# Kernel optimization log

Hardware: AMD Instinct MI355X
Metric: run time of the kernel (lower is better)

The kernel has to match this reference:

```python
import jax, jax.numpy as jnp
import numpy as np

N, E, H, L, IN, OUT = 50000, 600000, 128, 4, 10, 3
EPS = 1e-5

def _ln(x, g, b):
    m = jnp.mean(x, axis=-1, keepdims=True)
    v = jnp.mean(jnp.square(x - m), axis=-1, keepdims=True)
    return (x - m) * jax.lax.rsqrt(v + EPS) * g + b

def _mlp(x, w1, b1, w2, b2, g, be):
    h = jax.nn.relu(x @ w1 + b1)
    return _ln(h @ w2 + b2, g, be)

def setup_inputs() -> dict:
    key = jax.random.key(0)
    ks = iter(jax.random.split(key, 40))
    def w(shape, fan_in):
        return jax.random.normal(next(ks), shape, jnp.float32) * (1.0 / np.sqrt(fan_in))
    inp = {
        'x': jax.random.normal(next(ks), (N, IN), jnp.float32),
        'edge_index': jax.random.randint(next(ks), (2, E), 0, N, jnp.int32),
        'edge_attr': jax.random.normal(next(ks), (E, 3), jnp.float32),
        'enc_w1': w((IN, H), IN), 'enc_b1': jnp.zeros((H,), jnp.float32),
        'enc_w2': w((H, H), H), 'enc_b2': jnp.zeros((H,), jnp.float32),
        'enc_g': jnp.ones((H,), jnp.float32), 'enc_be': jnp.zeros((H,), jnp.float32),
        'edge_w1': w((L, 2 * H + 3, H), 2 * H + 3), 'edge_b1': jnp.zeros((L, H), jnp.float32),
        'edge_w2': w((L, H, H), H), 'edge_b2': jnp.zeros((L, H), jnp.float32),
        'edge_g': jnp.ones((L, H), jnp.float32), 'edge_be': jnp.zeros((L, H), jnp.float32),
        'node_w1': w((L, 2 * H, H), 2 * H), 'node_b1': jnp.zeros((L, H), jnp.float32),
        'node_w2': w((L, H, H), H), 'node_b2': jnp.zeros((L, H), jnp.float32),
        'node_g': jnp.ones((L, H), jnp.float32), 'node_be': jnp.zeros((L, H), jnp.float32),
        'dec_w1': w((H, H), H), 'dec_b1': jnp.zeros((H,), jnp.float32),
        'dec_w2': w((H, OUT), H), 'dec_b2': jnp.zeros((OUT,), jnp.float32),
    }
    return inp

def reference(x, edge_index, edge_attr,
              enc_w1, enc_b1, enc_w2, enc_b2, enc_g, enc_be,
              edge_w1, edge_b1, edge_w2, edge_b2, edge_g, edge_be,
              node_w1, node_b1, node_w2, node_b2, node_g, node_be,
              dec_w1, dec_b1, dec_w2, dec_b2):
    src, tgt = edge_index[0], edge_index[1]  # x_j = h[src], x_i = h[tgt]
    h = _mlp(x, enc_w1, enc_b1, enc_w2, enc_b2, enc_g, enc_be)  # [N,H]
    for l in range(L):
        x_i, x_j = h[tgt], h[src]                               # [E,H] gathers
        msg_in = jnp.concatenate([x_i, x_j, edge_attr], axis=1)  # [E,2H+3]
        msg = _mlp(msg_in, edge_w1[l], edge_b1[l], edge_w2[l], edge_b2[l], edge_g[l], edge_be[l])
        aggr = jax.ops.segment_sum(msg, tgt, num_segments=h.shape[0])  # [N,H]
        upd_in = jnp.concatenate([h, aggr], axis=1)              # [N,2H]
        h = h + _mlp(upd_in, node_w1[l], node_b1[l], node_w2[l], node_b2[l], node_g[l], node_be[l])
    out = jax.nn.relu(h @ dec_w1 + dec_b1) @ dec_w2 + dec_b2     # [N,OUT]
    return out
```

## Files before the change

kernel.cpp:

```cpp
#include <hip/hip_runtime.h>

#define H 128
#define LPAD 132
#define BM 64

typedef __attribute__((ext_vector_type(8))) short bf8;
typedef __attribute__((ext_vector_type(4))) float f4;
typedef __attribute__((ext_vector_type(4))) short s4;

__device__ __forceinline__ short f2bf(float f) {
    unsigned u = __float_as_uint(f);
    unsigned r = u + 0x7FFFu + ((u >> 16) & 1u);
    return (short)(r >> 16);
}
__device__ __forceinline__ float bf2f(unsigned lo16) {
    return __uint_as_float((lo16 & 0xFFFFu) << 16);
}

__global__ void pack_w(const float* __restrict__ W, short* __restrict__ out, int K, int KC) {
    const int layer = blockIdx.z;
    const float* Wl = W + (size_t)layer * K * H;
    short* ol = out + (size_t)layer * 8 * KC * 512;
    const int total = 8 * KC * 512;
    for (int idx = blockIdx.x * blockDim.x + threadIdx.x; idx < total; idx += gridDim.x * blockDim.x) {
        int i = idx & 7;
        int lane = (idx >> 3) & 63;
        int v = idx >> 9;
        int kc = v % KC;
        int m = v / KC;
        int k = kc * 32 + (lane >> 4) * 8 + i;
        int c = m * 16 + (lane & 15);
        float val = (k < K) ? Wl[(size_t)k * H + c] : 0.f;
        ol[idx] = f2bf(val);
    }
}

__global__ void pack_wts(const float* __restrict__ W , short* __restrict__ out) {
    const int layer = blockIdx.z;
    const float* Wl = W + (size_t)layer * 259 * 128;
    short* ol = out + (size_t)layer * 16 * 4 * 512;
    const int total = 16 * 4 * 512;
    for (int idx = blockIdx.x * blockDim.x + threadIdx.x; idx < total; idx += gridDim.x * blockDim.x) {
        int i = idx & 7;
        int lane = (idx >> 3) & 63;
        int v = idx >> 9;
        int kc = v & 3;
        int m = v >> 2;
        int k = kc * 32 + (lane >> 4) * 8 + i;
        int c = m * 16 + (lane & 15);
        float val = (c < 128) ? Wl[(size_t)k * 128 + c] : Wl[(size_t)(128 + k) * 128 + (c - 128)];
        ol[idx] = f2bf(val);
    }
}

__global__ void csr_count(const int* __restrict__ tgt, int* __restrict__ cnt, int E) {
    int e = blockIdx.x * blockDim.x + threadIdx.x;
    if (e < E) atomicAdd(&cnt[tgt[e]], 1);
}

#define SCAN_T 1024
__global__ __launch_bounds__(SCAN_T) void scan_excl(const int* __restrict__ cnt,
                                                    int* __restrict__ start, int n) {
    __shared__ int part[SCAN_T];
    int t = threadIdx.x;
    int chunk = (n + SCAN_T - 1) / SCAN_T;
    int lo = t * chunk, hi = min(lo + chunk, n);
    int s = 0;
    for (int i = lo; i < hi; ++i) s += cnt[i];
    part[t] = s;
    __syncthreads();
    for (int off = 1; off < SCAN_T; off <<= 1) {
        int v = (t >= off) ? part[t - off] : 0;
        __syncthreads();
        part[t] += v;
        __syncthreads();
    }
    int base = (t > 0) ? part[t - 1] : 0;
    for (int i = lo; i < hi; ++i) { start[i] = base; base += cnt[i]; }
}

__global__ void csr_scatter_reorder(const int* __restrict__ tgtI, const int* __restrict__ srcI,
                                    const float* __restrict__ eattr,
                                    int* __restrict__ start,
                                    int2* __restrict__ stpair,
                                    short* __restrict__ attrb, int E) {
    int e = blockIdx.x * blockDim.x + threadIdx.x;
    if (e >= E) return;
    int t = tgtI[e];
    int p = atomicAdd(&start[t], 1);
    stpair[p] = make_int2(srcI[e], t);
    s4 vv = {};
    vv[0] = f2bf(eattr[(size_t)e * 3 + 0]);
    vv[1] = f2bf(eattr[(size_t)e * 3 + 1]);
    vv[2] = f2bf(eattr[(size_t)e * 3 + 2]);
    *(s4*)(attrb + (size_t)p * 4) = vv;
}

__global__ __launch_bounds__(512, 4) void ts_mfma(
    const short* __restrict__ hbf, const short* __restrict__ wtsp,
    const float* __restrict__ b1,
    short* __restrict__ Tarr, short* __restrict__ Sarr,
    float* __restrict__ aggr, int N) {
    __shared__ __align__(16) short sW[16 * 4 * 512];
    const int tid = threadIdx.x;
    for (int t = tid; t < 16 * 4 * 512 / 8; t += 512) ((uint4*)sW)[t] = ((const uint4*)wtsp)[t];
    __syncthreads();

    const int lane = tid & 63;
    const int wv = tid >> 6;
    const int g = lane >> 4;
    const int er = lane & 15;
    const int n = blockIdx.x * 128 + wv * 16 + er;
    const int nC = (n < N) ? n : 0;
    const bf8* rT = (const bf8*)(hbf + (size_t)nC * H);

    f4 acc[16] = {};
#pragma unroll
    for (int kc = 0; kc < 4; ++kc) {
        bf8 b = rT[kc * 4 + g];
#pragma unroll
        for (int m = 0; m < 16; ++m)
            acc[m] = __builtin_amdgcn_mfma_f32_16x16x32_bf16(
                *(const bf8*)(sW + ((m * 4 + kc) * 64 + lane) * 8), b, acc[m], 0, 0, 0);
    }
    if (n >= N) return;
    short* oT = Tarr + (size_t)n * 128;
    short* oS = Sarr + (size_t)n * 128;
    float* oZ = aggr + (size_t)n * 128;
    const f4 zz = {0.f, 0.f, 0.f, 0.f};
#pragma unroll
    for (int m = 0; m < 16; ++m) {
        f4 v = acc[m];
        if (m < 8) {
            f4 bb = *(const f4*)(b1 + m * 16 + 4 * g);
            v = v + bb;
            *(f4*)(oZ + m * 16 + 4 * g) = zz;
        }
        unsigned p0, p1;
        asm("v_cvt_pk_bf16_f32 %0, %1, %2" : "=v"(p0) : "v"(v[0]), "v"(v[1]));
        asm("v_cvt_pk_bf16_f32 %0, %1, %2" : "=v"(p1) : "v"(v[2]), "v"(v[3]));
        uint2 uu; uu.x = p0; uu.y = p1;
        if (m < 8) *(uint2*)(oT + m * 16 + 4 * g) = uu;
        else       *(uint2*)(oS + (m - 8) * 16 + 4 * g) = uu;
    }
}

__global__ __launch_bounds__(512, 4) void edge_fused(
    const short* __restrict__ Tarr, const short* __restrict__ Sarr,
    const short* __restrict__ attrbf,
    const int2* __restrict__ stpair,
    const short* __restrict__ w2p,
    const float* __restrict__ w1aG,
    const float* __restrict__ b2,
    const float* __restrict__ gamma, const float* __restrict__ beta,
    float* __restrict__ aggr, int nrows) {
    __shared__ __align__(16) short sW2[8 * 4 * 512];
    __shared__ float sw1a[3 * 128];
    __shared__ __align__(16) unsigned smsg[128 * 64];
    __shared__ int stgt[128];

    const int tid = threadIdx.x;
    for (int t = tid; t < 8 * 4 * 512 / 8; t += 512) ((uint4*)sW2)[t] = ((const uint4*)w2p)[t];
    if (tid < 384) sw1a[tid] = w1aG[tid];
    const int e0b = blockIdx.x * 128;
    if (tid < 128) {
        int ee = e0b + tid;
        stgt[tid] = (ee < nrows) ? stpair[ee].y : -1;
    }
    __syncthreads();

    const int lane = tid & 63;
    const int wv = tid >> 6;
    const int g = lane >> 4;
    const int er = lane & 15;
    const int le = wv * 16 + er;
    const int e = e0b + le;
    const bool valid = e < nrows;
    const int eC = valid ? e : 0;
    const int2 st = stpair[eC];
    const int tS = st.x;
    const int tT = st.y;

    uint2 au = *(const uint2*)(attrbf + (size_t)eC * 4);
    const float at0 = bf2f(au.x), at1 = bf2f(au.x >> 16), at2 = bf2f(au.y);

    const short* Tp = Tarr + (size_t)tT * 128;
    const short* Sp = Sarr + (size_t)tS * 128;

    f4 acc2[8] = {};
#pragma unroll
    for (int kc2 = 0; kc2 < 4; ++kc2) {
        const int c0 = kc2 * 32 + 8 * g;
        uint4 tu = *(const uint4*)(Tp + c0);
        uint4 su = *(const uint4*)(Sp + c0);
        unsigned tw[4] = {tu.x, tu.y, tu.z, tu.w};
        unsigned swd[4] = {su.x, su.y, su.z, su.w};
        float hv[8];
#pragma unroll
        for (int p = 0; p < 4; ++p) {
            int j0 = 2 * p;
            float t0 = bf2f(tw[p]), t1 = bf2f(tw[p] >> 16);
            float s0 = bf2f(swd[p]), s1 = bf2f(swd[p] >> 16);
            float a = t0 + s0 + at0 * sw1a[c0 + j0] + at1 * sw1a[128 + c0 + j0] + at2 * sw1a[256 + c0 + j0];
            hv[j0] = fmaxf(a, 0.f);
            float b = t1 + s1 + at0 * sw1a[c0 + j0 + 1] + at1 * sw1a[128 + c0 + j0 + 1] + at2 * sw1a[256 + c0 + j0 + 1];
            hv[j0 + 1] = fmaxf(b, 0.f);
        }
        bf8 bfr;
        unsigned* bu = (unsigned*)&bfr;
#pragma unroll
        for (int p = 0; p < 4; ++p)
            asm("v_cvt_pk_bf16_f32 %0, %1, %2" : "=v"(bu[p]) : "v"(hv[2 * p]), "v"(hv[2 * p + 1]));
#pragma unroll
        for (int m = 0; m < 8; ++m)
            acc2[m] = __builtin_amdgcn_mfma_f32_16x16x32_bf16(
                *(const bf8*)(sW2 + ((m * 4 + kc2) * 64 + lane) * 8), bfr, acc2[m], 0, 0, 0);
    }

    float o[8][4];
    float s = 0.f, q = 0.f;
#pragma unroll
    for (int m = 0; m < 8; ++m) {
        f4 bb = *(const f4*)(b2 + m * 16 + 4 * g);
#pragma unroll
        for (int r = 0; r < 4; ++r) {
            float v = acc2[m][r] + bb[r];
            o[m][r] = v; s += v; q += v * v;
        }
    }
    s += __shfl_xor(s, 16, 64); q += __shfl_xor(q, 16, 64);
    s += __shfl_xor(s, 32, 64); q += __shfl_xor(q, 32, 64);
    const float mean = s * (1.f / 128.f);
    const float inv = rsqrtf(q * (1.f / 128.f) - mean * mean + 1e-5f);

    const unsigned swz = (unsigned)((le & 7) << 3);
    unsigned* row = smsg + le * 64;
#pragma unroll
    for (int m = 0; m < 8; ++m) {
        f4 gg = *(const f4*)(gamma + m * 16 + 4 * g);
        f4 be4 = *(const f4*)(beta + m * 16 + 4 * g);
        float v0 = valid ? ((o[m][0] - mean) * inv * gg[0] + be4[0]) : 0.f;
        float v1 = valid ? ((o[m][1] - mean) * inv * gg[1] + be4[1]) : 0.f;
        float v2 = valid ? ((o[m][2] - mean) * inv * gg[2] + be4[2]) : 0.f;
        float v3 = valid ? ((o[m][3] - mean) * inv * gg[3] + be4[3]) : 0.f;
        unsigned p0, p1;
        asm("v_cvt_pk_bf16_f32 %0, %1, %2" : "=v"(p0) : "v"(v0), "v"(v1));
        asm("v_cvt_pk_bf16_f32 %0, %1, %2" : "=v"(p1) : "v"(v2), "v"(v3));
        unsigned d0 = ((unsigned)(m * 8 + 2 * g)) ^ swz;
        uint2 uu; uu.x = p0; uu.y = p1;
        *(uint2*)(row + d0) = uu;
    }
    __syncthreads();

    const int c2 = tid & 63;
    const int chunk = tid >> 6;
    float a0 = 0.f, a1 = 0.f;
    int cur = stgt[chunk * 16];
    for (int j = 0; j < 16; ++j) {
        int le2 = chunk * 16 + j;
        int tg = stgt[le2];
        if (tg != cur) {
            if (cur >= 0) {
                atomicAdd(&aggr[(size_t)cur * 128 + 2 * c2], a0);
                atomicAdd(&aggr[(size_t)cur * 128 + 2 * c2 + 1], a1);
            }
            a0 = 0.f; a1 = 0.f; cur = tg;
        }
        unsigned u = smsg[le2 * 64 + (c2 ^ ((le2 & 7) << 3))];
        a0 += __uint_as_float(u << 16);
        a1 += __uint_as_float(u & 0xFFFF0000u);
    }
    if (cur >= 0) {
        atomicAdd(&aggr[(size_t)cur * 128 + 2 * c2], a0);
        atomicAdd(&aggr[(size_t)cur * 128 + 2 * c2 + 1], a1);
    }
}

__global__ __launch_bounds__(1024, 4) void node_mfma(
    const short* __restrict__ hbf, const float* __restrict__ aggrf,
    const short* __restrict__ w1p, const short* __restrict__ w2p,
    const float* __restrict__ b1, const float* __restrict__ b2,
    const float* __restrict__ gamma, const float* __restrict__ beta,
    float* __restrict__ outp, short* __restrict__ hbfout, int nrows) {
    __shared__ __align__(16) short sW1[8 * 8 * 512];
    __shared__ __align__(16) short sW2[8 * 4 * 512];

    const int tid = threadIdx.x;
    for (int t = tid; t < 8 * 8 * 512 / 8; t += 1024) ((uint4*)sW1)[t] = ((const uint4*)w1p)[t];
    for (int t = tid; t < 8 * 4 * 512 / 8; t += 1024) ((uint4*)sW2)[t] = ((const uint4*)w2p)[t];
    __syncthreads();

    const int lane = tid & 63;
    const int wv = tid >> 6;
    const int g = lane >> 4;
    const int er = lane & 15;
    const int e = blockIdx.x * 256 + wv * 16 + er;
    const bool valid = e < nrows;
    const int eC = valid ? e : 0;

    const bf8* rT = (const bf8*)(hbf + (size_t)eC * H);
    const f4* ra = (const f4*)(aggrf + (size_t)eC * H);

    f4 acc1[8] = {};
#pragma unroll
    for (int kc = 0; kc < 4; ++kc) {
        bf8 b = rT[kc * 4 + g];
#pragma unroll
        for (int m = 0; m < 8; ++m)
            acc1[m] = __builtin_amdgcn_mfma_f32_16x16x32_bf16(
                *(const bf8*)(sW1 + ((m * 8 + kc) * 64 + lane) * 8), b, acc1[m], 0, 0, 0);
    }
#pragma unroll
    for (int kc = 4; kc < 8; ++kc) {
        f4 a0 = ra[(kc - 4) * 8 + g * 2];
        f4 a1 = ra[(kc - 4) * 8 + g * 2 + 1];
        bf8 b;
        unsigned* bu = (unsigned*)&b;
        asm("v_cvt_pk_bf16_f32 %0, %1, %2" : "=v"(bu[0]) : "v"(a0[0]), "v"(a0[1]));
        asm("v_cvt_pk_bf16_f32 %0, %1, %2" : "=v"(bu[1]) : "v"(a0[2]), "v"(a0[3]));
        asm("v_cvt_pk_bf16_f32 %0, %1, %2" : "=v"(bu[2]) : "v"(a1[0]), "v"(a1[1]));
        asm("v_cvt_pk_bf16_f32 %0, %1, %2" : "=v"(bu[3]) : "v"(a1[2]), "v"(a1[3]));
#pragma unroll
        for (int m = 0; m < 8; ++m)
            acc1[m] = __builtin_amdgcn_mfma_f32_16x16x32_bf16(
                *(const bf8*)(sW1 + ((m * 8 + kc) * 64 + lane) * 8), b, acc1[m], 0, 0, 0);
    }

    float h1[8][4];
#pragma unroll
    for (int m = 0; m < 8; ++m) {
        f4 bb = *(const f4*)(b1 + m * 16 + 4 * g);
#pragma unroll
        for (int r = 0; r < 4; ++r) h1[m][r] = fmaxf(acc1[m][r] + bb[r], 0.f);
    }

    unsigned pk[8][2];
#pragma unroll
    for (int m = 0; m < 8; ++m)
#pragma unroll
        for (int hh = 0; hh < 2; ++hh)
            asm("v_cvt_pk_bf16_f32 %0, %1, %2"
                : "=v"(pk[m][hh]) : "v"(h1[m][2 * hh]), "v"(h1[m][2 * hh + 1]));

    f4 acc2[8] = {};
#pragma unroll
    for (int kc2 = 0; kc2 < 4; ++kc2) {
        bf8 bfr;
        unsigned* bu = (unsigned*)&bfr;
#pragma unroll
        for (int p = 0; p < 4; ++p) {
            int sl = er + 16 * (2 * (g & 1) + (p >> 1));
            unsigned lo = (unsigned)__shfl((int)pk[2 * kc2 + 0][p & 1], sl, 64);
            unsigned hi = (unsigned)__shfl((int)pk[2 * kc2 + 1][p & 1], sl, 64);
            bu[p] = (g >> 1) ? hi : lo;
        }
#pragma unroll
        for (int m = 0; m < 8; ++m)
            acc2[m] = __builtin_amdgcn_mfma_f32_16x16x32_bf16(
                *(const bf8*)(sW2 + ((m * 4 + kc2) * 64 + lane) * 8), bfr, acc2[m], 0, 0, 0);
    }

    float o[8][4];
    float s = 0.f, q = 0.f;
#pragma unroll
    for (int m = 0; m < 8; ++m) {
        f4 bb = *(const f4*)(b2 + m * 16 + 4 * g);
#pragma unroll
        for (int r = 0; r < 4; ++r) {
            float v = acc2[m][r] + bb[r];
            o[m][r] = v; s += v; q += v * v;
        }
    }
    s += __shfl_xor(s, 16, 64); q += __shfl_xor(q, 16, 64);
    s += __shfl_xor(s, 32, 64); q += __shfl_xor(q, 32, 64);
    const float mean = s * (1.f / 128.f);
    const float inv = rsqrtf(q * (1.f / 128.f) - mean * mean + 1e-5f);

    if (!valid) return;
    float* hp = outp + (size_t)eC * H;
    short* hb = hbfout + (size_t)eC * H;
#pragma unroll
    for (int m = 0; m < 8; ++m) {
        f4 gg = *(const f4*)(gamma + m * 16 + 4 * g);
        f4 be4 = *(const f4*)(beta + m * 16 + 4 * g);
        f4 hv = *(const f4*)(hp + m * 16 + 4 * g);
        f4 nv; s4 pkk;
#pragma unroll
        for (int r = 0; r < 4; ++r) {
            nv[r] = hv[r] + (o[m][r] - mean) * inv * gg[r] + be4[r];
            pkk[r] = f2bf(nv[r]);
        }
        *(f4*)(hp + m * 16 + 4 * g) = nv;
        *(s4*)(hb + m * 16 + 4 * g) = pkk;
    }
}

enum { MODE_ENC = 0, MODE_DEC = 3 };

__device__ __forceinline__ void fma_row(float acc[4], float a, const float4& b) {
    acc[0] = fmaf(a, b.x, acc[0]);
    acc[1] = fmaf(a, b.y, acc[1]);
    acc[2] = fmaf(a, b.z, acc[2]);
    acc[3] = fmaf(a, b.w, acc[3]);
}

__device__ __forceinline__ void gemm_seg(const float (*A)[LPAD], int K,
                                         const float* __restrict__ B,
                                         int row0, int c0, float acc[8][4]) {
    int k = 0;
    for (; k + 4 <= K; k += 4) {
        float4 b0 = *(const float4*)(B + (size_t)(k + 0) * H + c0);
        float4 b1 = *(const float4*)(B + (size_t)(k + 1) * H + c0);
        float4 b2 = *(const float4*)(B + (size_t)(k + 2) * H + c0);
        float4 b3 = *(const float4*)(B + (size_t)(k + 3) * H + c0);
#pragma unroll
        for (int j = 0; j < 8; ++j) {
            float4 a = *(const float4*)(&A[row0 + j][k]);
            fma_row(acc[j], a.x, b0);
            fma_row(acc[j], a.y, b1);
            fma_row(acc[j], a.z, b2);
            fma_row(acc[j], a.w, b3);
        }
    }
    for (; k < K; ++k) {
        float4 bv = *(const float4*)(B + (size_t)k * H + c0);
#pragma unroll
        for (int j = 0; j < 8; ++j) fma_row(acc[j], A[row0 + j][k], bv);
    }
}

template <int MODE>
__global__ __launch_bounds__(256, 2) void mlp_small(
    const float* __restrict__ in0,
    const float* __restrict__ w1, const float* __restrict__ b1,
    const float* __restrict__ w2, const float* __restrict__ b2,
    const float* __restrict__ g, const float* __restrict__ be,
    float* __restrict__ outp, short* __restrict__ hbfout, int nrows) {
    __shared__ __align__(16) float sA[BM][LPAD];

    const int tid = threadIdx.x;
    const int tr = tid >> 5, tc = tid & 31;
    const int c0 = tc * 4, row0 = tr * 8;
    const int r0 = blockIdx.x * BM;

    if (MODE == MODE_ENC) {
        for (int idx = tid; idx < BM * 10; idx += 256) {
            int r = idx / 10, c = idx - 10 * (idx / 10);
            int n = r0 + r;
            sA[r][c] = (n < nrows) ? in0[(size_t)n * 10 + c] : 0.f;
        }
    } else {
        for (int idx = tid; idx < BM * 32; idx += 256) {
            int r = idx >> 5, qq = idx & 31;
            int n = r0 + r;
            float4 v0 = make_float4(0.f, 0.f, 0.f, 0.f);
            if (n < nrows) v0 = ((const float4*)in0)[(size_t)n * 32 + qq];
            *(float4*)&sA[r][qq * 4] = v0;
        }
    }
    __syncthreads();

    float acc[8][4];
    {
        float4 bb = *(const float4*)&b1[c0];
#pragma unroll
        for (int j = 0; j < 8; ++j) { acc[j][0] = bb.x; acc[j][1] = bb.y; acc[j][2] = bb.z; acc[j][3] = bb.w; }
    }
    gemm_seg(sA, (MODE == MODE_ENC) ? 10 : H, w1, row0, c0, acc);
#pragma unroll
    for (int j = 0; j < 8; ++j)
#pragma unroll
        for (int r = 0; r < 4; ++r) acc[j][r] = fmaxf(acc[j][r], 0.f);

    __syncthreads();
#pragma unroll
    for (int j = 0; j < 8; ++j)
        *(float4*)&sA[row0 + j][c0] = make_float4(acc[j][0], acc[j][1], acc[j][2], acc[j][3]);
    __syncthreads();

    if (MODE == MODE_DEC) {
        if (tid < BM * 3) {
            int r = tid / 3, o = tid - 3 * (tid / 3);
            int gr = r0 + r;
            float sv = b2[o];
            for (int i = 0; i < H; ++i) sv = fmaf(sA[r][i], w2[(size_t)i * 3 + o], sv);
            if (gr < nrows) outp[(size_t)gr * 3 + o] = sv;
        }
        return;
    }

    {
        float4 bb = *(const float4*)&b2[c0];
#pragma unroll
        for (int j = 0; j < 8; ++j) { acc[j][0] = bb.x; acc[j][1] = bb.y; acc[j][2] = bb.z; acc[j][3] = bb.w; }
    }
    gemm_seg(sA, H, w2, row0, c0, acc);

    float4 g4 = *(const float4*)&g[c0];
    float4 be4 = *(const float4*)&be[c0];
#pragma unroll
    for (int j = 0; j < 8; ++j) {
        float s = acc[j][0] + acc[j][1] + acc[j][2] + acc[j][3];
        float q = acc[j][0] * acc[j][0] + acc[j][1] * acc[j][1] +
                  acc[j][2] * acc[j][2] + acc[j][3] * acc[j][3];
#pragma unroll
        for (int m = 1; m < 32; m <<= 1) { s += __shfl_xor(s, m); q += __shfl_xor(q, m); }
        float mean = s * (1.0f / 128.0f);
        float inv = rsqrtf(q * (1.0f / 128.0f) - mean * mean + 1e-5f);
        int gr = r0 + row0 + j;
        if (gr >= nrows) continue;
        float v0 = (acc[j][0] - mean) * inv * g4.x + be4.x;
        float v1 = (acc[j][1] - mean) * inv * g4.y + be4.y;
        float v2 = (acc[j][2] - mean) * inv * g4.z + be4.z;
        float v3 = (acc[j][3] - mean) * inv * g4.w + be4.w;
        *(float4*)&outp[(size_t)gr * H + c0] = make_float4(v0, v1, v2, v3);
        s4 pk = {f2bf(v0), f2bf(v1), f2bf(v2), f2bf(v3)};
        *(s4*)&hbfout[(size_t)gr * H + c0] = pk;
    }
}

static inline size_t align16(size_t x) { return (x + 15) & ~(size_t)15; }

extern "C" void kernel_launch(void* const* d_in, const int* in_sizes, int n_in,
                              void* d_out, int out_size, void* d_ws, size_t ws_size,
                              hipStream_t stream) {
    const float* x       = (const float*)d_in[0];
    const int*   ei      = (const int*)d_in[1];
    const float* eattr   = (const float*)d_in[2];
    const float* enc_w1  = (const float*)d_in[3];
    const float* enc_b1  = (const float*)d_in[4];
    const float* enc_w2  = (const float*)d_in[5];
    const float* enc_b2  = (const float*)d_in[6];
    const float* enc_g   = (const float*)d_in[7];
    const float* enc_be  = (const float*)d_in[8];
    const float* edge_w1 = (const float*)d_in[9];
    const float* edge_b1 = (const float*)d_in[10];
    const float* edge_w2 = (const float*)d_in[11];
    const float* edge_b2 = (const float*)d_in[12];
    const float* edge_g  = (const float*)d_in[13];
    const float* edge_be = (const float*)d_in[14];
    const float* node_w1 = (const float*)d_in[15];
    const float* node_b1 = (const float*)d_in[16];
    const float* node_w2 = (const float*)d_in[17];
    const float* node_b2 = (const float*)d_in[18];
    const float* node_g  = (const float*)d_in[19];
    const float* node_be = (const float*)d_in[20];
    const float* dec_w1  = (const float*)d_in[21];
    const float* dec_b1  = (const float*)d_in[22];
    const float* dec_w2  = (const float*)d_in[23];
    const float* dec_b2  = (const float*)d_in[24];

    const int N = in_sizes[0] / 10;
    const int E = in_sizes[1] / 2;
    const int* srcI = ei;
    const int* tgtI = ei + E;

    char* base = (char*)d_ws;
    size_t off = 0;
    float* h     = (float*)(base + off); off = align16(off + (size_t)N * H * 4);
    float* aggr  = (float*)(base + off); off = align16(off + (size_t)N * H * 4);
    short* hbf   = (short*)(base + off); off = align16(off + (size_t)N * H * 2);
    short* Tarr  = (short*)(base + off); off = align16(off + (size_t)N * H * 2);
    short* Sarr  = (short*)(base + off); off = align16(off + (size_t)N * H * 2);
    short* attrb = (short*)(base + off); off = align16(off + (size_t)E * 4 * 2);
    short* ewtsp = (short*)(base + off); off = align16(off + (size_t)4 * 16 * 4 * 512 * 2);
    short* ew2p  = (short*)(base + off); off = align16(off + (size_t)4 * 8 * 4 * 512 * 2);
    short* nw1p  = (short*)(base + off); off = align16(off + (size_t)4 * 8 * 8 * 512 * 2);
    short* nw2p  = (short*)(base + off); off = align16(off + (size_t)4 * 8 * 4 * 512 * 2);
    int*   cnt   = (int*)(base + off);  off = align16(off + (size_t)N * 4);
    int*   startp= (int*)(base + off);  off = align16(off + (size_t)(N + 1) * 4);
    int2*  stpair= (int2*)(base + off); off = align16(off + (size_t)E * 8);

    pack_wts<<<dim3(64, 1, 4), 256, 0, stream>>>(edge_w1, ewtsp);
    pack_w<<<dim3(32, 1, 4), 256, 0, stream>>>(edge_w2, ew2p, H, 4);
    pack_w<<<dim3(64, 1, 4), 256, 0, stream>>>(node_w1, nw1p, 2 * H, 8);
    pack_w<<<dim3(32, 1, 4), 256, 0, stream>>>(node_w2, nw2p, H, 4);

    hipMemsetAsync(cnt, 0, (size_t)N * 4, stream);
    csr_count<<<(E + 255) / 256, 256, 0, stream>>>(tgtI, cnt, E);
    scan_excl<<<1, SCAN_T, 0, stream>>>(cnt, startp, N);
    csr_scatter_reorder<<<(E + 255) / 256, 256, 0, stream>>>(
        tgtI, srcI, eattr, startp, stpair, attrb, E);

    const int gN64 = (N + BM - 1) / BM;
    mlp_small<MODE_ENC><<<gN64, 256, 0, stream>>>(
        x, enc_w1, enc_b1, enc_w2, enc_b2, enc_g, enc_be, h, hbf, N);

    const int gTS = (N + 127) / 128;
    const int gEe = (E + 127) / 128;
    const int gNN = (N + 255) / 256;
    for (int l = 0; l < 4; ++l) {
        ts_mfma<<<gTS, 512, 0, stream>>>(
            hbf, ewtsp + (size_t)l * 16 * 4 * 512, edge_b1 + (size_t)l * H, Tarr, Sarr, aggr, N);
        const float* w1aG = edge_w1 + (size_t)l * 259 * 128 + 256 * 128;
        edge_fused<<<gEe, 512, 0, stream>>>(
            Tarr, Sarr, attrb, stpair, ew2p + (size_t)l * 8 * 4 * 512, w1aG,
            edge_b2 + (size_t)l * H, edge_g + (size_t)l * H, edge_be + (size_t)l * H,
            aggr, E);
        node_mfma<<<gNN, 1024, 0, stream>>>(
            hbf, aggr,
            nw1p + (size_t)l * 8 * 8 * 512, nw2p + (size_t)l * 8 * 4 * 512,
            node_b1 + (size_t)l * H, node_b2 + (size_t)l * H,
            node_g + (size_t)l * H, node_be + (size_t)l * H,
            h, hbf, N);
    }

    mlp_small<MODE_DEC><<<gN64, 256, 0, stream>>>(
        h, dec_w1, dec_b1, dec_w2, dec_b2, nullptr, nullptr, (float*)d_out, nullptr, N);
}
```

Baseline: 795.6 us.

## Fuse next-layer T/S projection into node update kernel, halve edge message LDS

The node update kernel now also computes the next layer's per-node source and target projections. It packs the new h in registers, reshuffles it into MFMA operand layout with lane shuffles, and writes Tarr/Sarr and zeroes aggr, which removes three separate ts_mfma launches and a re-read of hbf. The edge kernel's message staging buffer is halved by staging and reducing the 128 edges in two passes of 64 with an extra barrier, lowering LDS use to allow more occupancy. The trade-off is more registers in node_mfma and a race risk, because aggr is read and zeroed for the same rows within one thread.

Measured after the change: 895.7 us. 12.6% more time.

```diff
diff --git a/kernel.cpp b/kernel.cpp
--- a/kernel.cpp
+++ b/kernel.cpp
@@ -156,7 +156,7 @@
     float* __restrict__ aggr, int nrows) {
     __shared__ __align__(16) short sW2[8 * 4 * 512];
     __shared__ float sw1a[3 * 128];
-    __shared__ __align__(16) unsigned smsg[128 * 64];
+    __shared__ __align__(16) unsigned smsg[64 * 64];
     __shared__ int stgt[128];
 
     const int tid = threadIdx.x;
@@ -233,8 +233,7 @@
     const float mean = s * (1.f / 128.f);
     const float inv = rsqrtf(q * (1.f / 128.f) - mean * mean + 1e-5f);
 
-    const unsigned swz = (unsigned)((le & 7) << 3);
-    unsigned* row = smsg + le * 64;
+    unsigned pm[8][2];
 #pragma unroll
     for (int m = 0; m < 8; ++m) {
         f4 gg = *(const f4*)(gamma + m * 16 + 4 * g);
@@ -243,45 +242,61 @@
         float v1 = valid ? ((o[m][1] - mean) * inv * gg[1] + be4[1]) : 0.f;
         float v2 = valid ? ((o[m][2] - mean) * inv * gg[2] + be4[2]) : 0.f;
         float v3 = valid ? ((o[m][3] - mean) * inv * gg[3] + be4[3]) : 0.f;
-        unsigned p0, p1;
-        asm("v_cvt_pk_bf16_f32 %0, %1, %2" : "=v"(p0) : "v"(v0), "v"(v1));
-        asm("v_cvt_pk_bf16_f32 %0, %1, %2" : "=v"(p1) : "v"(v2), "v"(v3));
-        unsigned d0 = ((unsigned)(m * 8 + 2 * g)) ^ swz;
-        uint2 uu; uu.x = p0; uu.y = p1;
-        *(uint2*)(row + d0) = uu;
-    }
-    __syncthreads();
-
-    const int c2 = tid & 63;
-    const int chunk = tid >> 6;
-    float a0 = 0.f, a1 = 0.f;
-    int cur = stgt[chunk * 16];
-    for (int j = 0; j < 16; ++j) {
-        int le2 = chunk * 16 + j;
-        int tg = stgt[le2];
-        if (tg != cur) {
-            if (cur >= 0) {
-                atomicAdd(&aggr[(size_t)cur * 128 + 2 * c2], a0);
-                atomicAdd(&aggr[(size_t)cur * 128 + 2 * c2 + 1], a1);
+        asm("v_cvt_pk_bf16_f32 %0, %1, %2" : "=v"(pm[m][0]) : "v"(v0), "v"(v1));
+        asm("v_cvt_pk_bf16_f32 %0, %1, %2" : "=v"(pm[m][1]) : "v"(v2), "v"(v3));
+    }
+
+    const int myhalf = le >> 6;
+    const int rloc = le & 63;
+    const int c2 = lane;
+#pragma unroll
+    for (int hh = 0; hh < 2; ++hh) {
+        if (myhalf == hh) {
+            const unsigned swz = (unsigned)((rloc & 7) << 3);
+            unsigned* row = smsg + rloc * 64;
+#pragma unroll
+            for (int m = 0; m < 8; ++m) {
+                unsigned d0 = ((unsigned)(m * 8 + 2 * g)) ^ swz;
+                uint2 uu; uu.x = pm[m][0]; uu.y = pm[m][1];
+                *(uint2*)(row + d0) = uu;
             }
-            a0 = 0.f; a1 = 0.f; cur = tg;
-        }
-        unsigned u = smsg[le2 * 64 + (c2 ^ ((le2 & 7) << 3))];
-        a0 += __uint_as_float(u << 16);
-        a1 += __uint_as_float(u & 0xFFFF0000u);
-    }
-    if (cur >= 0) {
-        atomicAdd(&aggr[(size_t)cur * 128 + 2 * c2], a0);
-        atomicAdd(&aggr[(size_t)cur * 128 + 2 * c2 + 1], a1);
-    }
-}
-
+        }
+        __syncthreads();
+        float a0 = 0.f, a1 = 0.f;
+        int cur = stgt[hh * 64 + wv * 8];
+#pragma unroll
+        for (int j = 0; j < 8; ++j) {
+            int rl = wv * 8 + j;
+            int tg = stgt[hh * 64 + rl];
+            if (tg != cur) {
+                if (cur >= 0) {
+                    atomicAdd(&aggr[(size_t)cur * 128 + 2 * c2], a0);
+                    atomicAdd(&aggr[(size_t)cur * 128 + 2 * c2 + 1], a1);
+                }
+                a0 = 0.f; a1 = 0.f; cur = tg;
+            }
+            unsigned u = smsg[rl * 64 + (c2 ^ ((rl & 7) << 3))];
+            a0 += __uint_as_float(u << 16);
+            a1 += __uint_as_float(u & 0xFFFF0000u);
+        }
+        if (cur >= 0) {
+            atomicAdd(&aggr[(size_t)cur * 128 + 2 * c2], a0);
+            atomicAdd(&aggr[(size_t)cur * 128 + 2 * c2 + 1], a1);
+        }
+        if (hh == 0) __syncthreads();
+    }
+}
+
+template <int NEXT>
 __global__ __launch_bounds__(1024, 4) void node_mfma(
     const short* __restrict__ hbf, const float* __restrict__ aggrf,
     const short* __restrict__ w1p, const short* __restrict__ w2p,
     const float* __restrict__ b1, const float* __restrict__ b2,
     const float* __restrict__ gamma, const float* __restrict__ beta,
-    float* __restrict__ outp, short* __restrict__ hbfout, int nrows) {
+    float* __restrict__ outp, short* __restrict__ hbfout,
+    const short* __restrict__ wtsnext, const float* __restrict__ b1next,
+    short* __restrict__ TarrO, short* __restrict__ SarrO,
+    float* __restrict__ aggrZ, int nrows) {
     __shared__ __align__(16) short sW1[8 * 8 * 512];
     __shared__ __align__(16) short sW2[8 * 4 * 512];
 
@@ -376,22 +391,87 @@
     const float mean = s * (1.f / 128.f);
     const float inv = rsqrtf(q * (1.f / 128.f) - mean * mean + 1e-5f);
 
-    if (!valid) return;
     float* hp = outp + (size_t)eC * H;
     short* hb = hbfout + (size_t)eC * H;
+    unsigned pkh[8][2];
 #pragma unroll
     for (int m = 0; m < 8; ++m) {
         f4 gg = *(const f4*)(gamma + m * 16 + 4 * g);
         f4 be4 = *(const f4*)(beta + m * 16 + 4 * g);
-        f4 hv = *(const f4*)(hp + m * 16 + 4 * g);
-        f4 nv; s4 pkk;
-#pragma unroll
-        for (int r = 0; r < 4; ++r) {
+        f4 hv;
+        if (valid) hv = *(const f4*)(hp + m * 16 + 4 * g);
+        else hv = f4{0.f, 0.f, 0.f, 0.f};
+        f4 nv;
+#pragma unroll
+        for (int r = 0; r < 4; ++r)
             nv[r] = hv[r] + (o[m][r] - mean) * inv * gg[r] + be4[r];
-            pkk[r] = f2bf(nv[r]);
-        }
-        *(f4*)(hp + m * 16 + 4 * g) = nv;
-        *(s4*)(hb + m * 16 + 4 * g) = pkk;
+        asm("v_cvt_pk_bf16_f32 %0, %1, %2" : "=v"(pkh[m][0]) : "v"(nv[0]), "v"(nv[1]));
+        asm("v_cvt_pk_bf16_f32 %0, %1, %2" : "=v"(pkh[m][1]) : "v"(nv[2]), "v"(nv[3]));
+        if (valid) {
+            *(f4*)(hp + m * 16 + 4 * g) = nv;
+            if (NEXT) {
+                uint2 uu; uu.x = pkh[m][0]; uu.y = pkh[m][1];
+                *(uint2*)(hb + m * 16 + 4 * g) = uu;
+            }
+        }
+    }
+
+    if (NEXT) {
+        bf8 bfrs[4];
+#pragma unroll
+        for (int kc = 0; kc < 4; ++kc) {
+            unsigned* bu = (unsigned*)&bfrs[kc];
+#pragma unroll
+            for (int p = 0; p < 4; ++p) {
+                int sl = er + 16 * (2 * (g & 1) + (p >> 1));
+                unsigned lo = (unsigned)__shfl((int)pkh[2 * kc + 0][p & 1], sl, 64);
+                unsigned hi = (unsigned)__shfl((int)pkh[2 * kc + 1][p & 1], sl, 64);
+                bu[p] = (g >> 1) ? hi : lo;
+            }
+        }
+        const bf8* wN = (const bf8*)wtsnext + lane;
+        f4 accT[8] = {};
+#pragma unroll
+        for (int kc = 0; kc < 4; ++kc)
+#pragma unroll
+            for (int m = 0; m < 8; ++m)
+                accT[m] = __builtin_amdgcn_mfma_f32_16x16x32_bf16(
+                    wN[(m * 4 + kc) * 64], bfrs[kc], accT[m], 0, 0, 0);
+        if (valid) {
+            short* oT = TarrO + (size_t)eC * 128;
+            float* oZ = aggrZ + (size_t)eC * 128;
+            const f4 zz = {0.f, 0.f, 0.f, 0.f};
+#pragma unroll
+            for (int m = 0; m < 8; ++m) {
+                f4 bb = *(const f4*)(b1next + m * 16 + 4 * g);
+                f4 v = accT[m] + bb;
+                unsigned p0, p1;
+                asm("v_cvt_pk_bf16_f32 %0, %1, %2" : "=v"(p0) : "v"(v[0]), "v"(v[1]));
+                asm("v_cvt_pk_bf16_f32 %0, %1, %2" : "=v"(p1) : "v"(v[2]), "v"(v[3]));
+                uint2 uu; uu.x = p0; uu.y = p1;
+                *(uint2*)(oT + m * 16 + 4 * g) = uu;
+                *(f4*)(oZ + m * 16 + 4 * g) = zz;
+            }
+        }
+        f4 accS[8] = {};
+#pragma unroll
+        for (int kc = 0; kc < 4; ++kc)
+#pragma unroll
+            for (int m = 0; m < 8; ++m)
+                accS[m] = __builtin_amdgcn_mfma_f32_16x16x32_bf16(
+                    wN[((m + 8) * 4 + kc) * 64], bfrs[kc], accS[m], 0, 0, 0);
+        if (valid) {
+            short* oS = SarrO + (size_t)eC * 128;
+#pragma unroll
+            for (int m = 0; m < 8; ++m) {
+                f4 v = accS[m];
+                unsigned p0, p1;
+                asm("v_cvt_pk_bf16_f32 %0, %1, %2" : "=v"(p0) : "v"(v[0]), "v"(v[1]));
+                asm("v_cvt_pk_bf16_f32 %0, %1, %2" : "=v"(p1) : "v"(v[2]), "v"(v[3]));
+                uint2 uu; uu.x = p0; uu.y = p1;
+                *(uint2*)(oS + m * 16 + 4 * g) = uu;
+            }
+        }
     }
 }
 
@@ -589,20 +669,34 @@
     const int gTS = (N + 127) / 128;
     const int gEe = (E + 127) / 128;
     const int gNN = (N + 255) / 256;
+
+    ts_mfma<<<gTS, 512, 0, stream>>>(
+        hbf, ewtsp, edge_b1, Tarr, Sarr, aggr, N);
+
     for (int l = 0; l < 4; ++l) {
-        ts_mfma<<<gTS, 512, 0, stream>>>(
-            hbf, ewtsp + (size_t)l * 16 * 4 * 512, edge_b1 + (size_t)l * H, Tarr, Sarr, aggr, N);
         const float* w1aG = edge_w1 + (size_t)l * 259 * 128 + 256 * 128;
         edge_fused<<<gEe, 512, 0, stream>>>(
             Tarr, Sarr, attrb, stpair, ew2p + (size_t)l * 8 * 4 * 512, w1aG,
             edge_b2 + (size_t)l * H, edge_g + (size_t)l * H, edge_be + (size_t)l * H,
             aggr, E);
-        node_mfma<<<gNN, 1024, 0, stream>>>(
-            hbf, aggr,
-            nw1p + (size_t)l * 8 * 8 * 512, nw2p + (size_t)l * 8 * 4 * 512,
-            node_b1 + (size_t)l * H, node_b2 + (size_t)l * H,
-            node_g + (size_t)l * H, node_be + (size_t)l * H,
-            h, hbf, N);
+        if (l < 3) {
+            node_mfma<1><<<gNN, 1024, 0, stream>>>(
+                hbf, aggr,
+                nw1p + (size_t)l * 8 * 8 * 512, nw2p + (size_t)l * 8 * 4 * 512,
+                node_b1 + (size_t)l * H, node_b2 + (size_t)l * H,
+                node_g + (size_t)l * H, node_be + (size_t)l * H,
+                h, hbf,
+                ewtsp + (size_t)(l + 1) * 16 * 4 * 512, edge_b1 + (size_t)(l + 1) * H,
+                Tarr, Sarr, aggr, N);
+        } else {
+            node_mfma<0><<<gNN, 1024, 0, stream>>>(
+                hbf, aggr,
+                nw1p + (size_t)l * 8 * 8 * 512, nw2p + (size_t)l * 8 * 4 * 512,
+                node_b1 + (size_t)l * H, node_b2 + (size_t)l * H,
+                node_g + (size_t)l * H, node_be + (size_t)l * H,
+                h, hbf,
+                nullptr, nullptr, nullptr, nullptr, nullptr, N);
+        }
     }
 
     mlp_small<MODE_DEC><<<gN64, 256, 0, stream>>>(
```
